# Kernel tuning notes

Measured on AMD Instinct MI355X. Metric: run time of the kernel, lower is better.

Reference implementation:

```python
import jax, jax.numpy as jnp
import numpy as np

S, B, E, H = 2048, 4, 1024, 16
D = E // H  # head_dim = 64


def setup_inputs() -> dict:
    key = jax.random.key(0)
    k1, k2, k3 = jax.random.split(key, 3)
    # xavier-uniform-ish init scales
    query = jax.random.normal(k1, (S, B, E), dtype=jnp.float32)
    in_proj_weight = jax.random.normal(k2, (3 * E, E), dtype=jnp.float32) * (2.0 / (4 * E)) ** 0.5
    in_proj_bias = jnp.zeros((3 * E,), dtype=jnp.float32)
    out_proj_weight = jax.random.normal(k3, (E, E), dtype=jnp.float32) * (1.0 / E) ** 0.5
    out_proj_bias = jnp.zeros((E,), dtype=jnp.float32)
    return {
        "query": query,
        "in_proj_weight": in_proj_weight,
        "in_proj_bias": in_proj_bias,
        "out_proj_weight": out_proj_weight,
        "out_proj_bias": out_proj_bias,
    }


def reference(query, in_proj_weight, in_proj_bias, out_proj_weight, out_proj_bias):
    # Self-attention path (qkv_same): fused in_proj then chunk into q,k,v.
    # query: (S, B, E); F.linear(x, W, b) = x @ W.T + b
    qkv = jnp.einsum('sbe,fe->sbf', query, in_proj_weight) + in_proj_bias  # (S, B, 3E)
    q, k, v = jnp.split(qkv, 3, axis=-1)  # each (S, B, E)
    scaling = D ** (-0.5)
    q = q * scaling
    # reshape to (B*H, S, D): view(S, B*H, D).transpose(0,1)
    def to_bh(x):
        return x.reshape(S, B * H, D).transpose(1, 0, 2)
    q, k, v = to_bh(q), to_bh(k), to_bh(v)
    # scores: (B*H, S, S)
    scores = jnp.einsum('nqd,nkd->nqk', q, k)
    attn = jax.nn.softmax(scores, axis=-1)  # dropout p=0 (inference)
    out = jnp.einsum('nqk,nkd->nqd', attn, v)  # (B*H, S, D)
    out = out.transpose(1, 0, 2).reshape(S, B, E)
    out = jnp.einsum('sbe,fe->sbf', out, out_proj_weight) + out_proj_bias
    return out
```

## Files before the change

kernel.cpp:

```cpp
#include <hip/hip_runtime.h>
#include <hip/hip_bf16.h>


typedef __attribute__((ext_vector_type(8))) short bf16x8;
typedef __attribute__((ext_vector_type(4))) float floatx4;

#define S_LEN 2048
#define EMB   1024
#define DHEAD 64

static __device__ __forceinline__ unsigned short f2bf(float x) {
    return __builtin_bit_cast(unsigned short, __float2bfloat16(x));
}

static __device__ __forceinline__ unsigned pack_bf16(float a, float b) {
    return (unsigned)f2bf(a) | ((unsigned)f2bf(b) << 16);
}

static __device__ __forceinline__ void dma16(const void* g, void* l) {
    __builtin_amdgcn_global_load_lds(
        (const __attribute__((address_space(1))) unsigned int*)(unsigned long long)g,
        (__attribute__((address_space(3))) unsigned int*)(unsigned int)(unsigned long long)l,
        16, 0, 0);
}

__global__ void detect_kernel(const unsigned short* __restrict__ q, int* __restrict__ flag) {
    __shared__ int cnt;
    if (threadIdx.x == 0) cnt = 0;
    __syncthreads();
    int local = 0;
    for (int i = threadIdx.x; i < 4096; i += 256) {
        unsigned short u = q[i];
        int e = (u >> 7) & 0xFF;
        if (e >= 132) local++;
    }
    atomicAdd(&cnt, local);
    __syncthreads();
    if (threadIdx.x == 0) *flag = (cnt > 100) ? 1 : 0;
}

__global__ void convert_all_kernel(
    const void* __restrict__ s0, const void* __restrict__ s1, const void* __restrict__ s2,
    const void* __restrict__ s3, const void* __restrict__ s4,
    __hip_bfloat16* __restrict__ d0, __hip_bfloat16* __restrict__ d1, __hip_bfloat16* __restrict__ d2,
    __hip_bfloat16* __restrict__ d3, __hip_bfloat16* __restrict__ d4,
    const int* __restrict__ flag)
{
    const int mode = *flag;
    const int c0 = 2097152, c1 = c0 + 786432, c2 = c1 + 768, c3 = c2 + 262144, c4 = c3 + 256;
    int i = blockIdx.x * blockDim.x + threadIdx.x;
    const int stride = gridDim.x * blockDim.x;
    for (; i < c4; i += stride) {
        const void* s; __hip_bfloat16* d; int off;
        if (i < c0)      { s = s0; d = d0; off = i; }
        else if (i < c1) { s = s1; d = d1; off = i - c0; }
        else if (i < c2) { s = s2; d = d2; off = i - c1; }
        else if (i < c3) { s = s3; d = d3; off = i - c2; }
        else             { s = s4; d = d4; off = i - c3; }
        if (mode) {
            float4 v = ((const float4*)s)[off];
            ushort4 o;
            o.x = f2bf(v.x); o.y = f2bf(v.y); o.z = f2bf(v.z); o.w = f2bf(v.w);
            ((ushort4*)d)[off] = o;
        } else {
            ((ushort4*)d)[off] = ((const ushort4*)s)[off];
        }
    }
}

#define GEMM_STAGE(As, Bs, Aptr, Bptr, ldA, ldB)                                       \
    {                                                                                  \
        const int srow = (l >> 3);                                                     \
        const int cG   = ((l & 7) ^ srow) * 8;                                         \
        _Pragma("unroll")                                                              \
        for (int j = 0; j < 4; j++) {                                                  \
            const int r0 = wave * 32 + j * 8;                                          \
            dma16(Aptr + (size_t)(r0 + srow) * ldA + cG, &As[r0][0]);                  \
            dma16(Bptr + (size_t)(r0 + srow) * ldB + cG, &Bs[r0][0]);                  \
        }                                                                              \
    }

__global__ __launch_bounds__(256) void qkv_gemm_kernel(
    const __hip_bfloat16* __restrict__ X,
    const __hip_bfloat16* __restrict__ W,
    const __hip_bfloat16* __restrict__ bias,
    __hip_bfloat16* __restrict__ Qws,
    __hip_bfloat16* __restrict__ Kws,
    __hip_bfloat16* __restrict__ Vws)
{
    __shared__ alignas(16) __hip_bfloat16 As[128][64];
    __shared__ alignas(16) __hip_bfloat16 Bs[128][64];

    const int t    = threadIdx.x;
    const int l    = t & 63;
    const int wave = t >> 6;
    const int l15  = l & 15;
    const int quad = l >> 4;
    const int wr   = (wave >> 1) * 64;
    const int wc   = (wave & 1) * 64;
    const int rowBase = blockIdx.x * 128;
    const int colBase = blockIdx.y * 128;

    floatx4 acc[4][4] = {};

    for (int k0 = 0; k0 < EMB; k0 += 64) {
        __syncthreads();
        const __hip_bfloat16* Ap = X + (size_t)rowBase * EMB + k0;
        const __hip_bfloat16* Bp = W + (size_t)colBase * EMB + k0;
        GEMM_STAGE(As, Bs, Ap, Bp, EMB, EMB)
        __syncthreads();
#pragma unroll
        for (int ks = 0; ks < 2; ks++) {
            bf16x8 af[4], bfr[4];
#pragma unroll
            for (int ti = 0; ti < 4; ti++) {
                const int rA = wr + ti * 16 + l15;
                af[ti] = *(const bf16x8*)(&As[rA][(((ks * 4 + quad) ^ (rA & 7)) * 8)]);
            }
#pragma unroll
            for (int tj = 0; tj < 4; tj++) {
                const int rB = wc + tj * 16 + l15;
                bfr[tj] = *(const bf16x8*)(&Bs[rB][(((ks * 4 + quad) ^ (rB & 7)) * 8)]);
            }
#pragma unroll
            for (int ti = 0; ti < 4; ti++)
#pragma unroll
                for (int tj = 0; tj < 4; tj++)
                    acc[ti][tj] = __builtin_amdgcn_mfma_f32_16x16x32_bf16(
                        af[ti], bfr[tj], acc[ti][tj], 0, 0, 0);
        }
    }

    const float QSCALE = 0.125f * 1.44269504088896f;
#pragma unroll
    for (int tj = 0; tj < 4; tj++) {
        const int col = colBase + wc + tj * 16 + l15;
        const int sec = col >> 10;
        const int e   = col & 1023;
        const int h   = e >> 6;
        const int d   = e & 63;
        const float bv = __bfloat162float(bias[col]);
#pragma unroll
        for (int ti = 0; ti < 4; ti++) {
#pragma unroll
            for (int r = 0; r < 4; r++) {
                const int row = rowBase + wr + ti * 16 + quad * 4 + r;
                const int s  = row >> 2;
                const int b  = row & 3;
                const int nh = b * 16 + h;
                const float val = acc[ti][tj][r] + bv;
                if (sec == 0) {
                    Qws[((size_t)nh * S_LEN + s) * DHEAD + d] = __float2bfloat16(val * QSCALE);
                } else if (sec == 1) {
                    Kws[((size_t)nh * S_LEN + s) * DHEAD + d] = __float2bfloat16(val);
                } else {
                    Vws[((size_t)nh * DHEAD + d) * S_LEN + s] = __float2bfloat16(val);
                }
            }
        }
    }
}

__global__ __launch_bounds__(256, 4) void attn_kernel(
    const __hip_bfloat16* __restrict__ Qws,
    const __hip_bfloat16* __restrict__ Kws,
    const __hip_bfloat16* __restrict__ Vws,
    __hip_bfloat16* __restrict__ AOut)
{
    __shared__ alignas(16) __hip_bfloat16 Ks[64][64];
    __shared__ alignas(16) __hip_bfloat16 Vts[64][64];
    __shared__ alignas(16) __hip_bfloat16 Ps[4][32][72];
    __shared__ float Ls[4][32];

    const int n  = blockIdx.x;
    const int q0 = blockIdx.y * 128;
    const int t    = threadIdx.x;
    const int l    = t & 63;
    const int wave = t >> 6;
    const int l15  = l & 15;
    const int quad = l >> 4;

    bf16x8 qa[2][2];
#pragma unroll
    for (int qs = 0; qs < 2; qs++)
#pragma unroll
        for (int ks = 0; ks < 2; ks++)
            qa[qs][ks] = *(const bf16x8*)(Qws +
                ((size_t)n * S_LEN + q0 + wave * 32 + qs * 16 + l15) * DHEAD + ks * 32 + quad * 8);

    floatx4 o[2][4] = {};
    float lsum[2] = {};

    const int srow = (l >> 3);
    const int cG   = ((l & 7) ^ srow) * 8;

    for (int kt = 0; kt < 32; kt++) {
        __syncthreads();
        const int key0 = kt * 64;
#pragma unroll
        for (int j = 0; j < 2; j++) {
            const int r0 = wave * 16 + j * 8;
            dma16(Kws + ((size_t)n * S_LEN + key0 + r0 + srow) * DHEAD + cG, &Ks[r0][0]);
            dma16(Vws + ((size_t)n * DHEAD + r0 + srow) * S_LEN + key0 + cG, &Vts[r0][0]);
        }
        __syncthreads();

        floatx4 sacc[2][4] = {};
#pragma unroll
        for (int ks = 0; ks < 2; ks++) {
#pragma unroll
            for (int nt = 0; nt < 4; nt++) {
                const int rK = nt * 16 + l15;
                bf16x8 kb = *(const bf16x8*)(&Ks[rK][(((ks * 4 + quad) ^ (rK & 7)) * 8)]);
#pragma unroll
                for (int qs = 0; qs < 2; qs++)
                    sacc[qs][nt] = __builtin_amdgcn_mfma_f32_16x16x32_bf16(
                        kb, qa[qs][ks], sacc[qs][nt], 0, 0, 0);
            }
        }

#pragma unroll
        for (int qs = 0; qs < 2; qs++) {
#pragma unroll
            for (int nt = 0; nt < 4; nt++) {
                const float p0 = __builtin_amdgcn_exp2f(sacc[qs][nt][0]);
                const float p1 = __builtin_amdgcn_exp2f(sacc[qs][nt][1]);
                const float p2 = __builtin_amdgcn_exp2f(sacc[qs][nt][2]);
                const float p3 = __builtin_amdgcn_exp2f(sacc[qs][nt][3]);
                lsum[qs] += (p0 + p1) + (p2 + p3);
                uint2 w;
                w.x = pack_bf16(p0, p1);
                w.y = pack_bf16(p2, p3);
                *(uint2*)(&Ps[wave][qs * 16 + l15][nt * 16 + quad * 4]) = w;
            }
        }

        bf16x8 pa[2][2];
#pragma unroll
        for (int qs = 0; qs < 2; qs++)
#pragma unroll
            for (int ks = 0; ks < 2; ks++)
                pa[qs][ks] = *(const bf16x8*)(&Ps[wave][qs * 16 + l15][ks * 32 + quad * 8]);
#pragma unroll
        for (int ks = 0; ks < 2; ks++) {
#pragma unroll
            for (int nt = 0; nt < 4; nt++) {
                const int rV = nt * 16 + l15;
                bf16x8 vb = *(const bf16x8*)(&Vts[rV][(((ks * 4 + quad) ^ (rV & 7)) * 8)]);
#pragma unroll
                for (int qs = 0; qs < 2; qs++)
                    o[qs][nt] = __builtin_amdgcn_mfma_f32_16x16x32_bf16(
                        pa[qs][ks], vb, o[qs][nt], 0, 0, 0);
            }
        }
    }

#pragma unroll
    for (int qs = 0; qs < 2; qs++) {
        float dsum = lsum[qs] + __shfl_xor(lsum[qs], 16);
        dsum += __shfl_xor(dsum, 32);
        if (quad == 0) Ls[wave][qs * 16 + l15] = 1.0f / dsum;
    }

    const int bb  = n >> 4;
    const int h64 = (n & 15) * 64;
#pragma unroll
    for (int qs = 0; qs < 2; qs++) {
        const float4 lv = *(const float4*)(&Ls[wave][qs * 16 + quad * 4]);
#pragma unroll
        for (int r = 0; r < 4; r++) {
            const float linv = ((const float*)&lv)[r];
#pragma unroll
            for (int nt = 0; nt < 4; nt++) {
                const int q = q0 + wave * 32 + qs * 16 + quad * 4 + r;
                const int d = nt * 16 + l15;
                AOut[((size_t)q * 4 + bb) * EMB + h64 + d] = __float2bfloat16(o[qs][nt][r] * linv);
            }
        }
    }
}

__global__ __launch_bounds__(256) void out_gemm_kernel(
    const __hip_bfloat16* __restrict__ A,
    const __hip_bfloat16* __restrict__ W,
    const __hip_bfloat16* __restrict__ bias,
    void* __restrict__ out,
    const int* __restrict__ flag)
{
    __shared__ alignas(16) __hip_bfloat16 As[128][64];
    __shared__ alignas(16) __hip_bfloat16 Bs[128][64];

    const int t    = threadIdx.x;
    const int l    = t & 63;
    const int wave = t >> 6;
    const int l15  = l & 15;
    const int quad = l >> 4;
    const int wr   = (wave >> 1) * 64;
    const int wc   = (wave & 1) * 64;
    const int rowBase = blockIdx.x * 128;
    const int colBase = blockIdx.y * 128;
    const int mode = *flag;

    floatx4 acc[4][4] = {};

    for (int k0 = 0; k0 < EMB; k0 += 64) {
        __syncthreads();
        const __hip_bfloat16* Ap = A + (size_t)rowBase * EMB + k0;
        const __hip_bfloat16* Bp = W + (size_t)colBase * EMB + k0;
        GEMM_STAGE(As, Bs, Ap, Bp, EMB, EMB)
        __syncthreads();
#pragma unroll
        for (int ks = 0; ks < 2; ks++) {
            bf16x8 af[4], bfr[4];
#pragma unroll
            for (int ti = 0; ti < 4; ti++) {
                const int rA = wr + ti * 16 + l15;
                af[ti] = *(const bf16x8*)(&As[rA][(((ks * 4 + quad) ^ (rA & 7)) * 8)]);
            }
#pragma unroll
            for (int tj = 0; tj < 4; tj++) {
                const int rB = wc + tj * 16 + l15;
                bfr[tj] = *(const bf16x8*)(&Bs[rB][(((ks * 4 + quad) ^ (rB & 7)) * 8)]);
            }
#pragma unroll
            for (int ti = 0; ti < 4; ti++)
#pragma unroll
                for (int tj = 0; tj < 4; tj++)
                    acc[ti][tj] = __builtin_amdgcn_mfma_f32_16x16x32_bf16(
                        af[ti], bfr[tj], acc[ti][tj], 0, 0, 0);
        }
    }

#pragma unroll
    for (int tj = 0; tj < 4; tj++) {
        const int col = colBase + wc + tj * 16 + l15;
        const float bv = __bfloat162float(bias[col]);
#pragma unroll
        for (int ti = 0; ti < 4; ti++) {
#pragma unroll
            for (int r = 0; r < 4; r++) {
                const int row = rowBase + wr + ti * 16 + quad * 4 + r;
                const float val = acc[ti][tj][r] + bv;
                if (mode) {
                    ((float*)out)[(size_t)row * EMB + col] = val;
                } else {
                    ((__hip_bfloat16*)out)[(size_t)row * EMB + col] = __float2bfloat16(val);
                }
            }
        }
    }
}

extern "C" void kernel_launch(void* const* d_in, const int* in_sizes, int n_in,
                              void* d_out, int out_size, void* d_ws, size_t ws_size,
                              hipStream_t stream) {
    const void* query = d_in[0];
    const void* w_in  = d_in[1];
    const void* b_in  = d_in[2];
    const void* w_out = d_in[3];
    const void* b_out = d_in[4];

    char* ws = (char*)d_ws;
    int*            flag   = (int*)ws;
    __hip_bfloat16* Xc     = (__hip_bfloat16*)(ws + 256);
    __hip_bfloat16* Winc   = Xc   + (size_t)8192 * 1024;
    __hip_bfloat16* binc   = Winc + (size_t)3072 * 1024;
    __hip_bfloat16* Woutc  = binc + 3072;
    __hip_bfloat16* boutc  = Woutc + (size_t)1024 * 1024;
    __hip_bfloat16* Qws    = boutc + 1024;
    __hip_bfloat16* Kws    = Qws + (size_t)8388608;
    __hip_bfloat16* Vws    = Kws + (size_t)8388608;
    __hip_bfloat16* AOut   = Vws + (size_t)8388608;

    detect_kernel<<<1, 256, 0, stream>>>((const unsigned short*)query, flag);

    convert_all_kernel<<<2048, 256, 0, stream>>>(query, w_in, b_in, w_out, b_out,
                                                 Xc, Winc, binc, Woutc, boutc, flag);

    qkv_gemm_kernel<<<dim3(64, 24), 256, 0, stream>>>(Xc, Winc, binc, Qws, Kws, Vws);
    attn_kernel<<<dim3(64, 16), 256, 0, stream>>>(Qws, Kws, Vws, AOut);
    out_gemm_kernel<<<dim3(64, 8), 256, 0, stream>>>(AOut, Woutc, boutc, d_out, flag);
}
```

Before: 291.1 us.

## Remap GEMM tiles across XCDs and stage V-transpose stores through LDS

```diff
diff --git a/kernel.cpp b/kernel.cpp
--- a/kernel.cpp
+++ b/kernel.cpp
@@ -80,6 +80,13 @@
         }                                                                              \
     }
 
+#define XCD_SWIZZLE()                                                                  \
+    const int orig = blockIdx.x + blockIdx.y * gridDim.x;                              \
+    const int cpx  = (gridDim.x * gridDim.y) >> 3;                                     \
+    const int swz  = (orig & 7) * cpx + (orig >> 3);                                   \
+    const int rowBase = (swz & 63) * 128;                                              \
+    const int colBase = (swz >> 6) * 128;
+
 __global__ __launch_bounds__(256) void qkv_gemm_kernel(
     const __hip_bfloat16* __restrict__ X,
     const __hip_bfloat16* __restrict__ W,
@@ -88,8 +95,9 @@
     __hip_bfloat16* __restrict__ Kws,
     __hip_bfloat16* __restrict__ Vws)
 {
-    __shared__ alignas(16) __hip_bfloat16 As[128][64];
-    __shared__ alignas(16) __hip_bfloat16 Bs[128][64];
+    __shared__ alignas(16) __hip_bfloat16 SH[16384];
+    auto As = (__hip_bfloat16 (*)[64])(&SH[0]);
+    auto Bs = (__hip_bfloat16 (*)[64])(&SH[8192]);
 
     const int t    = threadIdx.x;
     const int l    = t & 63;
@@ -98,8 +106,7 @@
     const int quad = l >> 4;
     const int wr   = (wave >> 1) * 64;
     const int wc   = (wave & 1) * 64;
-    const int rowBase = blockIdx.x * 128;
-    const int colBase = blockIdx.y * 128;
+    XCD_SWIZZLE()
 
     floatx4 acc[4][4] = {};
 
@@ -132,29 +139,61 @@
     }
 
     const float QSCALE = 0.125f * 1.44269504088896f;
-#pragma unroll
-    for (int tj = 0; tj < 4; tj++) {
-        const int col = colBase + wc + tj * 16 + l15;
-        const int sec = col >> 10;
-        const int e   = col & 1023;
-        const int h   = e >> 6;
-        const int d   = e & 63;
-        const float bv = __bfloat162float(bias[col]);
-#pragma unroll
-        for (int ti = 0; ti < 4; ti++) {
-#pragma unroll
-            for (int r = 0; r < 4; r++) {
-                const int row = rowBase + wr + ti * 16 + quad * 4 + r;
-                const int s  = row >> 2;
-                const int b  = row & 3;
-                const int nh = b * 16 + h;
-                const float val = acc[ti][tj][r] + bv;
-                if (sec == 0) {
-                    Qws[((size_t)nh * S_LEN + s) * DHEAD + d] = __float2bfloat16(val * QSCALE);
-                } else if (sec == 1) {
-                    Kws[((size_t)nh * S_LEN + s) * DHEAD + d] = __float2bfloat16(val);
-                } else {
-                    Vws[((size_t)nh * DHEAD + d) * S_LEN + s] = __float2bfloat16(val);
+
+    if (colBase >= 2048) {
+        __syncthreads();
+        auto Ct = (__hip_bfloat16 (*)[128][32])(&SH[0]);
+#pragma unroll
+        for (int tj = 0; tj < 4; tj++) {
+            const int eloc = wc + tj * 16 + l15;
+            const float bv = __bfloat162float(bias[colBase + eloc]);
+#pragma unroll
+            for (int ti = 0; ti < 4; ti++) {
+                const int sidx = (wr >> 2) + ti * 4 + quad;
+#pragma unroll
+                for (int r = 0; r < 4; r++)
+                    Ct[r][eloc][sidx] = __float2bfloat16(acc[ti][tj][r] + bv);
+            }
+        }
+        __syncthreads();
+        const int e0 = colBase - 2048;
+        const int s0 = rowBase >> 2;
+#pragma unroll
+        for (int p = 0; p < 8; p++) {
+            const int slot = p * 256 + t;
+            const int seg  = slot >> 2;
+            const int q4   = slot & 3;
+            const int b    = seg >> 7;
+            const int eloc = seg & 127;
+            const int e    = e0 + eloc;
+            const int n    = b * 16 + (e >> 6);
+            const int d    = e & 63;
+            uint4 w = *(const uint4*)(&Ct[b][eloc][q4 * 8]);
+            *(uint4*)(Vws + ((size_t)n * DHEAD + d) * S_LEN + s0 + q4 * 8) = w;
+        }
+    } else {
+#pragma unroll
+        for (int tj = 0; tj < 4; tj++) {
+            const int col = colBase + wc + tj * 16 + l15;
+            const int sec = col >> 10;
+            const int e   = col & 1023;
+            const int h   = e >> 6;
+            const int d   = e & 63;
+            const float bv = __bfloat162float(bias[col]);
+#pragma unroll
+            for (int ti = 0; ti < 4; ti++) {
+#pragma unroll
+                for (int r = 0; r < 4; r++) {
+                    const int row = rowBase + wr + ti * 16 + quad * 4 + r;
+                    const int s  = row >> 2;
+                    const int b  = row & 3;
+                    const int nh = b * 16 + h;
+                    const float val = acc[ti][tj][r] + bv;
+                    if (sec == 0) {
+                        Qws[((size_t)nh * S_LEN + s) * DHEAD + d] = __float2bfloat16(val * QSCALE);
+                    } else {
+                        Kws[((size_t)nh * S_LEN + s) * DHEAD + d] = __float2bfloat16(val);
+                    }
                 }
             }
         }
@@ -297,8 +336,7 @@
     const int quad = l >> 4;
     const int wr   = (wave >> 1) * 64;
     const int wc   = (wave & 1) * 64;
-    const int rowBase = blockIdx.x * 128;
-    const int colBase = blockIdx.y * 128;
+    XCD_SWIZZLE()
     const int mode = *flag;
 
     floatx4 acc[4][4] = {};
```

Result: no change. 295.7 us (+1.6%).
